# Kernel optimization log

Measured on AMD Instinct MI355X. Metric: run time of the kernel, lower is better.

## Reference

```python
import jax, jax.numpy as jnp
import numpy as np
import math

EMB_DIM = 1024
HEAD_SIZE = 64
T = 4096
B = 4

def setup_inputs() -> dict:
    key = jax.random.key(0)
    k1, k2, k3, k4 = jax.random.split(key, 4)
    scale = 1.0 / math.sqrt(EMB_DIM)
    return {
        "input": jax.random.normal(k1, (B, T, EMB_DIM), dtype=jnp.float32),
        "Wq": jax.random.normal(k2, (EMB_DIM, HEAD_SIZE), dtype=jnp.float32) * scale,
        "Wk": jax.random.normal(k3, (EMB_DIM, HEAD_SIZE), dtype=jnp.float32) * scale,
        "Wv": jax.random.normal(k4, (EMB_DIM, HEAD_SIZE), dtype=jnp.float32) * scale,
    }

def reference(input, Wq, Wk, Wv):
    # q,k,v: [B,T,H]
    q = input @ Wq
    k = input @ Wk
    v = input @ Wv
    # scores: [B,T,T]
    match = jnp.einsum('bqh,bkh->bqk', q, k)
    # 'encoder' mask in this repo = causal tril mask
    causal = jnp.tril(jnp.ones((T, T), dtype=bool))
    match = jnp.where(causal, match, -jnp.inf)
    # NOTE: faithful to source quirk: softmax first, THEN divide by sqrt(head_size)
    attention = jax.nn.softmax(match, axis=-1) / math.sqrt(HEAD_SIZE)
    return jnp.einsum('bqk,bkh->bqh', attention, v)
```

## Files before the change

### kernel.cpp

```cpp
#include <hip/hip_runtime.h>

#define T_SEQ 4096
#define NBATCH 4
#define EMB 1024
#define HS 64
#define BT (NBATCH * T_SEQ)

typedef float f32x4 __attribute__((ext_vector_type(4)));
typedef short s16x8 __attribute__((ext_vector_type(8)));

__device__ __forceinline__ unsigned short f2bf(float x) {
  union { float f; unsigned u; } c; c.f = x;
  unsigned r = c.u + 0x7FFF + ((c.u >> 16) & 1);
  return (unsigned short)(r >> 16);
}
__device__ __forceinline__ float bf2f(unsigned short h) {
  union { unsigned u; float f; } c; c.u = ((unsigned)h) << 16;
  return c.f;
}
__device__ __forceinline__ unsigned cvtpk(float lo, float hi) {
  unsigned r;
  asm("v_cvt_pk_bf16_f32 %0, %1, %2" : "=v"(r) : "v"(lo), "v"(hi));
  return r;
}
__device__ __forceinline__ void cvt8(float4 a0, float4 a1, s16x8& hi, s16x8& lo) {
  float xv[8] = {a0.x, a0.y, a0.z, a0.w, a1.x, a1.y, a1.z, a1.w};
#pragma unroll
  for (int j = 0; j < 8; ++j) {
    unsigned short h = f2bf(xv[j]);
    hi[j] = (short)h;
    lo[j] = (short)f2bf(xv[j] - bf2f(h));
  }
}
__device__ __forceinline__ void cvt8t(float4 a0, float4 a1, s16x8& hi, s16x8& lo) {
  float xv[8] = {a0.x, a0.y, a0.z, a0.w, a1.x, a1.y, a1.z, a1.w};
  unsigned hu[8], lu[8];
#pragma unroll
  for (int j = 0; j < 8; ++j) {
    union { float f; unsigned u; } c; c.f = xv[j];
    hu[j] = c.u;
    union { unsigned u; float f; } hf; hf.u = c.u & 0xFFFF0000u;
    union { float f; unsigned u; } r; r.f = xv[j] - hf.f;
    lu[j] = r.u;
  }
  union { s16x8 v; unsigned u[4]; } H, L;
#pragma unroll
  for (int j = 0; j < 4; ++j) {
    H.u[j] = (hu[2 * j] >> 16) | (hu[2 * j + 1] & 0xFFFF0000u);
    L.u[j] = (lu[2 * j] >> 16) | (lu[2 * j + 1] & 0xFFFF0000u);
  }
  hi = H.v; lo = L.v;
}

__device__ __forceinline__ void gl16(const void* g, void* l) {
  __builtin_amdgcn_global_load_lds(
      (const __attribute__((address_space(1))) void*)g,
      (__attribute__((address_space(3))) void*)l, 16, 0, 0);
}

__global__ __launch_bounds__(256) void wconv(
    const float* __restrict__ Wq, const float* __restrict__ Wk,
    const float* __restrict__ Wv, unsigned short* __restrict__ wt_hi,
    unsigned short* __restrict__ wt_lo) {
  const int n3 = blockIdx.x;
  const int which = n3 >> 6, n = n3 & 63;
  const float* W = (which == 0) ? Wq : (which == 1) ? Wk : Wv;
#pragma unroll
  for (int i = 0; i < 4; ++i) {
    int k = i * 256 + threadIdx.x;
    float x = W[(size_t)k * HS + n];
    unsigned short h = f2bf(x);
    wt_hi[(size_t)n3 * EMB + k] = h;
    wt_lo[(size_t)n3 * EMB + k] = f2bf(x - bf2f(h));
  }
}

__global__ __launch_bounds__(512) void qkv_mfma(
    const float* __restrict__ inp, const unsigned short* __restrict__ wt_hi,
    const unsigned short* __restrict__ wt_lo, float* __restrict__ qf,
    unsigned short* __restrict__ khi, unsigned short* __restrict__ klo,
    unsigned short* __restrict__ vtb) {
  __shared__ __align__(16) unsigned short S0[24576];
  __shared__ __align__(16) unsigned short S1[24576];
  const int t = threadIdx.x, lane = t & 63, w = t >> 6;
  const int m = lane & 15, quad = lane >> 4;
  const int mg = w >> 1, ng = w & 1;
  const int tok0 = blockIdx.x * 64;
  const int arow = tok0 + mg * 16 + m;

  f32x4 acc[6];
#pragma unroll
  for (int nt = 0; nt < 6; ++nt) acc[nt] = (f32x4){0.f, 0.f, 0.f, 0.f};

  const int rl = lane >> 3;
  const int cl = ((lane & 7) ^ rl) * 8;
  const unsigned short* ghi = wt_hi + (size_t)(w * 8 + rl) * EMB + cl;
  const unsigned short* glo = wt_lo + (size_t)(w * 8 + rl) * EMB + cl;
  unsigned short* const l0 = S0 + w * 512;
  unsigned short* const l1 = S1 + w * 512;

#define SB0() __builtin_amdgcn_sched_barrier(0)

#define STAGE(LB, K0)                                    \
  gl16(ghi + (K0), (LB));                                \
  gl16(ghi + 64 * EMB + (K0), (LB) + 4096);              \
  gl16(ghi + 128 * EMB + (K0), (LB) + 8192);             \
  gl16(glo + (K0), (LB) + 12288);                        \
  gl16(glo + 64 * EMB + (K0), (LB) + 16384);             \
  gl16(glo + 128 * EMB + (K0), (LB) + 20480);            \
  SB0();

#define LOAD_A(K0, PA0, PA1, PA2, PA3)                               \
  {                                                                  \
    const float* ap = &inp[(size_t)arow * EMB + (K0) + quad * 8];    \
    PA0 = *(const float4*)ap;        PA1 = *(const float4*)(ap + 4); \
    PA2 = *(const float4*)(ap + 32); PA3 = *(const float4*)(ap + 36);\
  }

#define VMBAR(N)                                                        \
  {                                                                     \
    SB0();                                                              \
    asm volatile("s_waitcnt vmcnt(" #N ") lgkmcnt(0)" ::: "memory");    \
    SB0();                                                              \
    __builtin_amdgcn_s_barrier();                                       \
  }

  const int csw0 = (quad ^ (m & 7)) * 8;
  const int csw1 = ((quad + 4) ^ (m & 7)) * 8;

#define QKV_TILE(S, AH0, AL0, AH1, AL1)                                      \
  {                                                                          \
    _Pragma("unroll")                                                        \
    for (int nt = 0; nt < 6; ++nt) {                                         \
      const int bb = (ng * 96 + nt * 16 + m) * 64;                           \
      f32x4 a = acc[nt];                                                     \
      {                                                                      \
        s16x8 bh = *(const s16x8*)&S[bb + csw0];                             \
        s16x8 bl = *(const s16x8*)&S[12288 + bb + csw0];                     \
        a = __builtin_amdgcn_mfma_f32_16x16x32_bf16(AH0, bh, a, 0, 0, 0);    \
        a = __builtin_amdgcn_mfma_f32_16x16x32_bf16(AH0, bl, a, 0, 0, 0);    \
        a = __builtin_amdgcn_mfma_f32_16x16x32_bf16(AL0, bh, a, 0, 0, 0);    \
      }                                                                      \
      {                                                                      \
        s16x8 bh = *(const s16x8*)&S[bb + csw1];                             \
        s16x8 bl = *(const s16x8*)&S[12288 + bb + csw1];                     \
        a = __builtin_amdgcn_mfma_f32_16x16x32_bf16(AH1, bh, a, 0, 0, 0);    \
        a = __builtin_amdgcn_mfma_f32_16x16x32_bf16(AH1, bl, a, 0, 0, 0);    \
        a = __builtin_amdgcn_mfma_f32_16x16x32_bf16(AL1, bh, a, 0, 0, 0);    \
      }                                                                      \
      acc[nt] = a;                                                           \
    }                                                                        \
  }

  float4 paA0, paA1, paA2, paA3;
  float4 paB0, paB1, paB2, paB3;

  STAGE(l0, 0);
  LOAD_A(0, paA0, paA1, paA2, paA3);
  LOAD_A(64, paB0, paB1, paB2, paB3);
  VMBAR(8);

#pragma unroll 1
  for (int kc = 0; kc < 8; ++kc) {
    STAGE(l1, (2 * kc + 1) * 64);
    {
      s16x8 ah0, al0, ah1, al1;
      cvt8t(paA0, paA1, ah0, al0);
      cvt8t(paA2, paA3, ah1, al1);
      if (kc < 7) { LOAD_A((2 * kc + 2) * 64, paA0, paA1, paA2, paA3); }
      QKV_TILE(S0, ah0, al0, ah1, al1);
    }
    if (kc < 7) { VMBAR(4); } else { VMBAR(0); }
    if (kc < 7) { STAGE(l0, (2 * kc + 2) * 64); }
    {
      s16x8 ah0, al0, ah1, al1;
      cvt8t(paB0, paB1, ah0, al0);
      cvt8t(paB2, paB3, ah1, al1);
      if (kc < 7) { LOAD_A((2 * kc + 3) * 64, paB0, paB1, paB2, paB3); }
      QKV_TILE(S1, ah0, al0, ah1, al1);
    }
    if (kc < 7) VMBAR(4);
  }

#undef STAGE
#undef LOAD_A
#undef QKV_TILE
#undef VMBAR
#undef SB0

#pragma unroll
  for (int nt = 0; nt < 6; ++nt) {
    int n3 = ng * 96 + nt * 16 + m;
    int which = n3 >> 6, col = n3 & 63;
#pragma unroll
    for (int r = 0; r < 4; ++r) {
      int tok = tok0 + mg * 16 + quad * 4 + r;
      float val = acc[nt][r];
      if (which == 0) {
        qf[(size_t)tok * HS + col] = val * 1.44269504088896f;
      } else if (which == 1) {
        unsigned short h = f2bf(val);
        khi[(size_t)tok * HS + col] = h;
        klo[(size_t)tok * HS + col] = f2bf(val - bf2f(h));
      } else {
        vtb[(size_t)(tok >> 6) * 4096 + (size_t)col * 64 + (tok & 63)] = f2bf(val);
      }
    }
  }
}

__global__ __launch_bounds__(256) void attn_part(
    const float* __restrict__ q, const unsigned short* __restrict__ khi,
    const unsigned short* __restrict__ klo, const unsigned short* __restrict__ vt,
    unsigned short* __restrict__ partO, float* __restrict__ partML) {
  __shared__ unsigned short Khi_s[64 * 72];
  __shared__ unsigned short Klo_s[64 * 72];
  __shared__ unsigned short Vt_s[64 * 72];
  __shared__ unsigned short P_s[4 * 16 * 72];
  const int t = threadIdx.x;
  const int lane = t & 63, w = t >> 6;
  const int m = lane & 15, quad = lane >> 4;

  int u = blockIdx.x;
  const int b = u / 160;
  u -= b * 160;
  int qtile = 0, c = 0;
  {
    int acc2 = 0;
    for (int qq = 0; qq < 64; ++qq) {
      int ncq = (qq >> 4) + 1;
      if (u < acc2 + ncq) { qtile = qq; c = u - acc2; break; }
      acc2 += ncq;
    }
  }
  const int kt0 = c * 16;
  const int kt1 = (kt0 + 16 < qtile + 1) ? kt0 + 16 : qtile + 1;

  const size_t qrow0 = (size_t)b * T_SEQ + (size_t)qtile * 64;
  const size_t krowbase = (size_t)b * T_SEQ;
  const int q_loc = w * 16 + m;

  s16x8 qh[2], ql[2];
#pragma unroll
  for (int cc = 0; cc < 2; ++cc) {
    const float* qp = &q[(qrow0 + q_loc) * HS + cc * 32 + quad * 8];
    cvt8(*(const float4*)qp, *(const float4*)(qp + 4), qh[cc], ql[cc]);
  }

  float l_st = 0.f;
  f32x4 o[4];
#pragma unroll
  for (int hb = 0; hb < 4; ++hb) o[hb] = (f32x4){0.f, 0.f, 0.f, 0.f};

  const int r0 = t >> 3, ch0 = t & 7;
  const int r1 = (256 + t) >> 3, ch1 = t & 7;

  uint4 pk0h, pk0l, pv0, pk1h, pk1l, pv1;
  {
    size_t g0 = (krowbase + (size_t)kt0 * 64 + r0) * HS + ch0 * 8;
    size_t g1 = (krowbase + (size_t)kt0 * 64 + r1) * HS + ch1 * 8;
    pk0h = *(const uint4*)&khi[g0]; pk0l = *(const uint4*)&klo[g0];
    pk1h = *(const uint4*)&khi[g1]; pk1l = *(const uint4*)&klo[g1];
    size_t v0 = (size_t)(b * 64 + kt0) * 4096 + (size_t)r0 * 64 + ch0 * 8;
    size_t v1 = (size_t)(b * 64 + kt0) * 4096 + (size_t)r1 * 64 + ch1 * 8;
    pv0 = *(const uint4*)&vt[v0]; pv1 = *(const uint4*)&vt[v1];
  }

  for (int kt = kt0; kt < kt1; ++kt) {
    __syncthreads();
    *(uint4*)&Khi_s[r0 * 72 + ch0 * 8] = pk0h;
    *(uint4*)&Klo_s[r0 * 72 + ch0 * 8] = pk0l;
    *(uint4*)&Vt_s[r0 * 72 + ch0 * 8] = pv0;
    *(uint4*)&Khi_s[r1 * 72 + ch1 * 8] = pk1h;
    *(uint4*)&Klo_s[r1 * 72 + ch1 * 8] = pk1l;
    *(uint4*)&Vt_s[r1 * 72 + ch1 * 8] = pv1;
    __syncthreads();

    if (kt + 1 < kt1) {
      size_t g0 = (krowbase + (size_t)(kt + 1) * 64 + r0) * HS + ch0 * 8;
      size_t g1 = (krowbase + (size_t)(kt + 1) * 64 + r1) * HS + ch1 * 8;
      pk0h = *(const uint4*)&khi[g0]; pk0l = *(const uint4*)&klo[g0];
      pk1h = *(const uint4*)&khi[g1]; pk1l = *(const uint4*)&klo[g1];
      size_t v0 = (size_t)(b * 64 + kt + 1) * 4096 + (size_t)r0 * 64 + ch0 * 8;
      size_t v1 = (size_t)(b * 64 + kt + 1) * 4096 + (size_t)r1 * 64 + ch1 * 8;
      pv0 = *(const uint4*)&vt[v0]; pv1 = *(const uint4*)&vt[v1];
    }

    f32x4 st[4];
#pragma unroll
    for (int cb = 0; cb < 4; ++cb) {
      st[cb] = (f32x4){0.f, 0.f, 0.f, 0.f};
#pragma unroll
      for (int cc = 0; cc < 2; ++cc) {
        s16x8 bh = *(const s16x8*)&Khi_s[(cb * 16 + m) * 72 + cc * 32 + quad * 8];
        s16x8 bl = *(const s16x8*)&Klo_s[(cb * 16 + m) * 72 + cc * 32 + quad * 8];
        st[cb] = __builtin_amdgcn_mfma_f32_16x16x32_bf16(bh, qh[cc], st[cb], 0, 0, 0);
        st[cb] = __builtin_amdgcn_mfma_f32_16x16x32_bf16(bl, qh[cc], st[cb], 0, 0, 0);
        st[cb] = __builtin_amdgcn_mfma_f32_16x16x32_bf16(bh, ql[cc], st[cb], 0, 0, 0);
      }
    }
    if (kt == qtile) {
#pragma unroll
      for (int cb = 0; cb < 4; ++cb)
#pragma unroll
        for (int r = 0; r < 4; ++r)
          if (cb * 16 + quad * 4 + r > q_loc) st[cb][r] = -1e30f;
    }
    float tc[4];
#pragma unroll
    for (int cb = 0; cb < 4; ++cb) {
#pragma unroll
      for (int r = 0; r < 4; ++r) st[cb][r] = exp2f(st[cb][r]);
      tc[cb] = (st[cb][0] + st[cb][1]) + (st[cb][2] + st[cb][3]);
    }
    l_st += (tc[0] + tc[1]) + (tc[2] + tc[3]);
#pragma unroll
    for (int cb = 0; cb < 4; ++cb) {
      uint2 pk;
      pk.x = cvtpk(st[cb][0], st[cb][1]);
      pk.y = cvtpk(st[cb][2], st[cb][3]);
      *(uint2*)&P_s[q_loc * 72 + cb * 16 + quad * 4] = pk;
    }
    s16x8 pf[2];
#pragma unroll
    for (int cc = 0; cc < 2; ++cc)
      pf[cc] = *(const s16x8*)&P_s[q_loc * 72 + cc * 32 + quad * 8];
#pragma unroll
    for (int hb = 0; hb < 4; ++hb) {
#pragma unroll
      for (int cc = 0; cc < 2; ++cc) {
        s16x8 vf = *(const s16x8*)&Vt_s[(hb * 16 + m) * 72 + cc * 32 + quad * 8];
        o[hb] = __builtin_amdgcn_mfma_f32_16x16x32_bf16(vf, pf[cc], o[hb], 0, 0, 0);
      }
    }
  }

  l_st += __shfl_xor(l_st, 16, 64);
  l_st += __shfl_xor(l_st, 32, 64);

  const int slot = ((b * 64 + qtile) << 2) + c;
  unsigned short* Op = partO + (size_t)slot * 4096;
#pragma unroll
  for (int hb = 0; hb < 4; ++hb) {
    uint2 pk;
    pk.x = cvtpk(o[hb][0], o[hb][1]);
    pk.y = cvtpk(o[hb][2], o[hb][3]);
    *(uint2*)&Op[q_loc * 64 + hb * 16 + quad * 4] = pk;
  }
  if (quad == 0) partML[(size_t)slot * 64 + q_loc] = l_st;
}

__global__ __launch_bounds__(256) void attn_combine(
    const unsigned short* __restrict__ partO, const float* __restrict__ partML,
    float* __restrict__ out) {
  const int qtile = blockIdx.x, b = blockIdx.y;
  const int t = threadIdx.x;
  const int row = t >> 2, hg = t & 3;
  const int nc = (qtile >> 4) + 1;
  const int slot0 = (b * 64 + qtile) << 2;

  float lsum = 0.f;
  for (int i = 0; i < nc; ++i) lsum += partML[(size_t)(slot0 + i) * 64 + row];
  const float inv = 1.f / (lsum * 8.0f);

  float acc[16];
#pragma unroll
  for (int e = 0; e < 16; ++e) acc[e] = 0.f;
  for (int i = 0; i < nc; ++i) {
    const unsigned short* Op =
        partO + (size_t)(slot0 + i) * 4096 + row * 64 + hg * 16;
    uint4 u0 = *(const uint4*)Op;
    uint4 u1 = *(const uint4*)(Op + 8);
    unsigned uv[8] = {u0.x, u0.y, u0.z, u0.w, u1.x, u1.y, u1.z, u1.w};
#pragma unroll
    for (int e = 0; e < 8; ++e) {
      acc[2 * e] += bf2f((unsigned short)(uv[e] & 0xFFFF));
      acc[2 * e + 1] += bf2f((unsigned short)(uv[e] >> 16));
    }
  }
  float* op = &out[((size_t)b * T_SEQ + (size_t)qtile * 64 + row) * HS + hg * 16];
#pragma unroll
  for (int v = 0; v < 4; ++v) {
    float4 r;
    r.x = acc[4 * v + 0] * inv; r.y = acc[4 * v + 1] * inv;
    r.z = acc[4 * v + 2] * inv; r.w = acc[4 * v + 3] * inv;
    ((float4*)op)[v] = r;
  }
}

extern "C" void kernel_launch(void* const* d_in, const int* in_sizes, int n_in,
                              void* d_out, int out_size, void* d_ws, size_t ws_size,
                              hipStream_t stream) {
  const float* inp = (const float*)d_in[0];
  const float* Wq  = (const float*)d_in[1];
  const float* Wk  = (const float*)d_in[2];
  const float* Wv  = (const float*)d_in[3];
  float* out = (float*)d_out;

  char* base = (char*)d_ws;
  float* qf = (float*)base;
  unsigned short* khi = (unsigned short*)(base + (size_t)BT * HS * 4);
  unsigned short* klo = khi + (size_t)BT * HS;
  unsigned short* vtb = klo + (size_t)BT * HS;
  unsigned short* wt_hi = vtb + (size_t)BT * HS;
  unsigned short* wt_lo = wt_hi + (size_t)192 * EMB;
  unsigned short* partO = wt_lo + (size_t)192 * EMB;
  float* partML = (float*)(partO + (size_t)1024 * 4096);

  wconv<<<dim3(192), dim3(256), 0, stream>>>(Wq, Wk, Wv, wt_hi, wt_lo);
  qkv_mfma<<<dim3(BT / 64), dim3(512), 0, stream>>>(inp, wt_hi, wt_lo, qf, khi, klo, vtb);
  attn_part<<<dim3(640), dim3(256), 0, stream>>>(qf, khi, klo, vtb, partO, partML);
  attn_combine<<<dim3(64, NBATCH), dim3(256), 0, stream>>>(partO, partML, out);
}
```

Before: 166.0 us.

## Double-buffer K/V tiles in LDS via direct global-to-LDS loads with XOR swizzle

Replaces the register-staged single LDS buffer with two LDS buffers filled by direct global-to-LDS loads (gl16). The next tile is prefetched while the current one is computed, and each step needs only one barrier instead of two. The padded layout becomes an XOR-swizzled layout to avoid bank conflicts, and blocks are launched in reverse order so the heavy causal tiles start first. LDS use roughly doubles, which may lower occupancy, and the correctness of the swizzle and the ordering relies on sched_barrier placement.

```diff
diff --git a/kernel.cpp b/kernel.cpp
--- a/kernel.cpp
+++ b/kernel.cpp
@@ -213,15 +213,14 @@
     const float* __restrict__ q, const unsigned short* __restrict__ khi,
     const unsigned short* __restrict__ klo, const unsigned short* __restrict__ vt,
     unsigned short* __restrict__ partO, float* __restrict__ partML) {
-  __shared__ unsigned short Khi_s[64 * 72];
-  __shared__ unsigned short Klo_s[64 * 72];
-  __shared__ unsigned short Vt_s[64 * 72];
+  __shared__ __align__(16) unsigned short S0[12288];
+  __shared__ __align__(16) unsigned short S1[12288];
   __shared__ unsigned short P_s[4 * 16 * 72];
   const int t = threadIdx.x;
   const int lane = t & 63, w = t >> 6;
   const int m = lane & 15, quad = lane >> 4;
 
-  int u = blockIdx.x;
+  int u = (int)gridDim.x - 1 - blockIdx.x;
   const int b = u / 160;
   u -= b * 160;
   int qtile = 0, c = 0;
@@ -252,88 +251,115 @@
 #pragma unroll
   for (int hb = 0; hb < 4; ++hb) o[hb] = (f32x4){0.f, 0.f, 0.f, 0.f};
 
-  const int r0 = t >> 3, ch0 = t & 7;
-  const int r1 = (256 + t) >> 3, ch1 = t & 7;
-
-  uint4 pk0h, pk0l, pv0, pk1h, pk1l, pv1;
-  {
-    size_t g0 = (krowbase + (size_t)kt0 * 64 + r0) * HS + ch0 * 8;
-    size_t g1 = (krowbase + (size_t)kt0 * 64 + r1) * HS + ch1 * 8;
-    pk0h = *(const uint4*)&khi[g0]; pk0l = *(const uint4*)&klo[g0];
-    pk1h = *(const uint4*)&khi[g1]; pk1l = *(const uint4*)&klo[g1];
-    size_t v0 = (size_t)(b * 64 + kt0) * 4096 + (size_t)r0 * 64 + ch0 * 8;
-    size_t v1 = (size_t)(b * 64 + kt0) * 4096 + (size_t)r1 * 64 + ch1 * 8;
-    pv0 = *(const uint4*)&vt[v0]; pv1 = *(const uint4*)&vt[v1];
-  }
-
-  for (int kt = kt0; kt < kt1; ++kt) {
-    __syncthreads();
-    *(uint4*)&Khi_s[r0 * 72 + ch0 * 8] = pk0h;
-    *(uint4*)&Klo_s[r0 * 72 + ch0 * 8] = pk0l;
-    *(uint4*)&Vt_s[r0 * 72 + ch0 * 8] = pv0;
-    *(uint4*)&Khi_s[r1 * 72 + ch1 * 8] = pk1h;
-    *(uint4*)&Klo_s[r1 * 72 + ch1 * 8] = pk1l;
-    *(uint4*)&Vt_s[r1 * 72 + ch1 * 8] = pv1;
-    __syncthreads();
-
+  const int lro = lane >> 3;
+  const int lcs = ((lane & 7) ^ lro) * 8;
+  const int rloc = w * 16 + lro;
+  const unsigned short* pkh = khi + (krowbase + rloc) * HS + lcs;
+  const unsigned short* pkl = klo + (krowbase + rloc) * HS + lcs;
+  const unsigned short* pvt = vt + (size_t)(b * 64) * 4096 + rloc * 64 + lcs;
+
+#define SB0() __builtin_amdgcn_sched_barrier(0)
+#define STAGE(SB, KT)                                        \
+  {                                                          \
+    const size_t o_ = (size_t)(KT) * 4096;                   \
+    gl16(pkh + o_,       (SB) + w * 1024);                   \
+    gl16(pkh + o_ + 512, (SB) + w * 1024 + 512);             \
+    gl16(pkl + o_,       (SB) + 4096 + w * 1024);            \
+    gl16(pkl + o_ + 512, (SB) + 4096 + w * 1024 + 512);      \
+    gl16(pvt + o_,       (SB) + 8192 + w * 1024);            \
+    gl16(pvt + o_ + 512, (SB) + 8192 + w * 1024 + 512);      \
+    SB0();                                                   \
+  }
+#define VMBAR0()                                                      \
+  {                                                                   \
+    SB0();                                                            \
+    asm volatile("s_waitcnt vmcnt(0) lgkmcnt(0)" ::: "memory");       \
+    SB0();                                                            \
+    __builtin_amdgcn_s_barrier();                                     \
+  }
+
+  const int rc0 = ((quad)     ^ (m & 7)) * 8;
+  const int rc1 = ((quad + 4) ^ (m & 7)) * 8;
+
+#define ACOMPUTE(SB, KT)                                                       \
+  {                                                                            \
+    f32x4 st[4];                                                               \
+    _Pragma("unroll")                                                          \
+    for (int cb = 0; cb < 4; ++cb) {                                           \
+      st[cb] = (f32x4){0.f, 0.f, 0.f, 0.f};                                    \
+      const int rb = (cb * 16 + m) * 64;                                       \
+      {                                                                        \
+        s16x8 bh = *(const s16x8*)&(SB)[rb + rc0];                             \
+        s16x8 bl = *(const s16x8*)&(SB)[4096 + rb + rc0];                      \
+        st[cb] = __builtin_amdgcn_mfma_f32_16x16x32_bf16(bh, qh[0], st[cb], 0, 0, 0); \
+        st[cb] = __builtin_amdgcn_mfma_f32_16x16x32_bf16(bl, qh[0], st[cb], 0, 0, 0); \
+        st[cb] = __builtin_amdgcn_mfma_f32_16x16x32_bf16(bh, ql[0], st[cb], 0, 0, 0); \
+      }                                                                        \
+      {                                                                        \
+        s16x8 bh = *(const s16x8*)&(SB)[rb + rc1];                             \
+        s16x8 bl = *(const s16x8*)&(SB)[4096 + rb + rc1];                      \
+        st[cb] = __builtin_amdgcn_mfma_f32_16x16x32_bf16(bh, qh[1], st[cb], 0, 0, 0); \
+        st[cb] = __builtin_amdgcn_mfma_f32_16x16x32_bf16(bl, qh[1], st[cb], 0, 0, 0); \
+        st[cb] = __builtin_amdgcn_mfma_f32_16x16x32_bf16(bh, ql[1], st[cb], 0, 0, 0); \
+      }                                                                        \
+    }                                                                          \
+    if ((KT) == qtile) {                                                       \
+      _Pragma("unroll")                                                        \
+      for (int cb = 0; cb < 4; ++cb)                                           \
+        _Pragma("unroll")                                                      \
+        for (int r = 0; r < 4; ++r)                                            \
+          if (cb * 16 + quad * 4 + r > q_loc) st[cb][r] = -1e30f;              \
+    }                                                                          \
+    float tc[4];                                                               \
+    _Pragma("unroll")                                                          \
+    for (int cb = 0; cb < 4; ++cb) {                                           \
+      _Pragma("unroll")                                                        \
+      for (int r = 0; r < 4; ++r) st[cb][r] = exp2f(st[cb][r]);                \
+      tc[cb] = (st[cb][0] + st[cb][1]) + (st[cb][2] + st[cb][3]);              \
+    }                                                                          \
+    l_st += (tc[0] + tc[1]) + (tc[2] + tc[3]);                                 \
+    _Pragma("unroll")                                                          \
+    for (int cb = 0; cb < 4; ++cb) {                                           \
+      uint2 pk;                                                                \
+      pk.x = cvtpk(st[cb][0], st[cb][1]);                                      \
+      pk.y = cvtpk(st[cb][2], st[cb][3]);                                      \
+      *(uint2*)&P_s[q_loc * 72 + cb * 16 + quad * 4] = pk;                     \
+    }                                                                          \
+    s16x8 pf0 = *(const s16x8*)&P_s[q_loc * 72 + quad * 8];                    \
+    s16x8 pf1 = *(const s16x8*)&P_s[q_loc * 72 + 32 + quad * 8];               \
+    _Pragma("unroll")                                                          \
+    for (int hb = 0; hb < 4; ++hb) {                                           \
+      const int vb = (hb * 16 + m) * 64;                                       \
+      {                                                                        \
+        s16x8 vf = *(const s16x8*)&(SB)[8192 + vb + rc0];                      \
+        o[hb] = __builtin_amdgcn_mfma_f32_16x16x32_bf16(vf, pf0, o[hb], 0, 0, 0); \
+      }                                                                        \
+      {                                                                        \
+        s16x8 vf = *(const s16x8*)&(SB)[8192 + vb + rc1];                      \
+        o[hb] = __builtin_amdgcn_mfma_f32_16x16x32_bf16(vf, pf1, o[hb], 0, 0, 0); \
+      }                                                                        \
+    }                                                                          \
+  }
+
+  STAGE(S0, kt0);
+  VMBAR0();
+
+#pragma unroll 1
+  for (int kt = kt0; kt < kt1; kt += 2) {
+    if (kt + 1 < kt1) STAGE(S1, kt + 1);
+    ACOMPUTE(S0, kt);
+    VMBAR0();
     if (kt + 1 < kt1) {
-      size_t g0 = (krowbase + (size_t)(kt + 1) * 64 + r0) * HS + ch0 * 8;
-      size_t g1 = (krowbase + (size_t)(kt + 1) * 64 + r1) * HS + ch1 * 8;
-      pk0h = *(const uint4*)&khi[g0]; pk0l = *(const uint4*)&klo[g0];
-      pk1h = *(const uint4*)&khi[g1]; pk1l = *(const uint4*)&klo[g1];
-      size_t v0 = (size_t)(b * 64 + kt + 1) * 4096 + (size_t)r0 * 64 + ch0 * 8;
-      size_t v1 = (size_t)(b * 64 + kt + 1) * 4096 + (size_t)r1 * 64 + ch1 * 8;
-      pv0 = *(const uint4*)&vt[v0]; pv1 = *(const uint4*)&vt[v1];
-    }
-
-    f32x4 st[4];
-#pragma unroll
-    for (int cb = 0; cb < 4; ++cb) {
-      st[cb] = (f32x4){0.f, 0.f, 0.f, 0.f};
-#pragma unroll
-      for (int cc = 0; cc < 2; ++cc) {
-        s16x8 bh = *(const s16x8*)&Khi_s[(cb * 16 + m) * 72 + cc * 32 + quad * 8];
-        s16x8 bl = *(const s16x8*)&Klo_s[(cb * 16 + m) * 72 + cc * 32 + quad * 8];
-        st[cb] = __builtin_amdgcn_mfma_f32_16x16x32_bf16(bh, qh[cc], st[cb], 0, 0, 0);
-        st[cb] = __builtin_amdgcn_mfma_f32_16x16x32_bf16(bl, qh[cc], st[cb], 0, 0, 0);
-        st[cb] = __builtin_amdgcn_mfma_f32_16x16x32_bf16(bh, ql[cc], st[cb], 0, 0, 0);
-      }
-    }
-    if (kt == qtile) {
-#pragma unroll
-      for (int cb = 0; cb < 4; ++cb)
-#pragma unroll
-        for (int r = 0; r < 4; ++r)
-          if (cb * 16 + quad * 4 + r > q_loc) st[cb][r] = -1e30f;
-    }
-    float tc[4];
-#pragma unroll
-    for (int cb = 0; cb < 4; ++cb) {
-#pragma unroll
-      for (int r = 0; r < 4; ++r) st[cb][r] = exp2f(st[cb][r]);
-      tc[cb] = (st[cb][0] + st[cb][1]) + (st[cb][2] + st[cb][3]);
-    }
-    l_st += (tc[0] + tc[1]) + (tc[2] + tc[3]);
-#pragma unroll
-    for (int cb = 0; cb < 4; ++cb) {
-      uint2 pk;
-      pk.x = cvtpk(st[cb][0], st[cb][1]);
-      pk.y = cvtpk(st[cb][2], st[cb][3]);
-      *(uint2*)&P_s[q_loc * 72 + cb * 16 + quad * 4] = pk;
-    }
-    s16x8 pf[2];
-#pragma unroll
-    for (int cc = 0; cc < 2; ++cc)
-      pf[cc] = *(const s16x8*)&P_s[q_loc * 72 + cc * 32 + quad * 8];
-#pragma unroll
-    for (int hb = 0; hb < 4; ++hb) {
-#pragma unroll
-      for (int cc = 0; cc < 2; ++cc) {
-        s16x8 vf = *(const s16x8*)&Vt_s[(hb * 16 + m) * 72 + cc * 32 + quad * 8];
-        o[hb] = __builtin_amdgcn_mfma_f32_16x16x32_bf16(vf, pf[cc], o[hb], 0, 0, 0);
-      }
-    }
-  }
+      if (kt + 2 < kt1) STAGE(S0, kt + 2);
+      ACOMPUTE(S1, kt + 1);
+      VMBAR0();
+    }
+  }
+
+#undef STAGE
+#undef VMBAR0
+#undef ACOMPUTE
+#undef SB0
 
   l_st += __shfl_xor(l_st, 16, 64);
   l_st += __shfl_xor(l_st, 32, 64);
```

After: 173.2 us. +4.4%, slower.

## Enlarge attention query tile to 128 rows with 512-thread blocks

Applied to the files above, without the earlier changes.

Doubles the query rows per attention block from 64 to 128 using 8 waves, so each K/V tile staged in shared memory is reused by twice as many queries. Grid shrinks from 640 to 320 blocks, and the combine kernel is adapted to the new partial layout. This halves K/V global and LDS load traffic per query, at the cost of fewer blocks, coarser causal load balance, and a second masked diagonal tile per block.

```diff
diff --git a/kernel.cpp b/kernel.cpp
--- a/kernel.cpp
+++ b/kernel.cpp
@@ -209,34 +209,35 @@
   }
 }
 
-__global__ __launch_bounds__(256) void attn_part(
+__global__ __launch_bounds__(512) void attn_part(
     const float* __restrict__ q, const unsigned short* __restrict__ khi,
     const unsigned short* __restrict__ klo, const unsigned short* __restrict__ vt,
     unsigned short* __restrict__ partO, float* __restrict__ partML) {
   __shared__ unsigned short Khi_s[64 * 72];
   __shared__ unsigned short Klo_s[64 * 72];
   __shared__ unsigned short Vt_s[64 * 72];
-  __shared__ unsigned short P_s[4 * 16 * 72];
+  __shared__ unsigned short P_s[128 * 72];
   const int t = threadIdx.x;
   const int lane = t & 63, w = t >> 6;
   const int m = lane & 15, quad = lane >> 4;
 
   int u = blockIdx.x;
-  const int b = u / 160;
-  u -= b * 160;
+  const int b = u / 80;
+  u -= b * 80;
   int qtile = 0, c = 0;
   {
     int acc2 = 0;
-    for (int qq = 0; qq < 64; ++qq) {
-      int ncq = (qq >> 4) + 1;
+    for (int qq = 0; qq < 32; ++qq) {
+      int ncq = (qq >> 3) + 1;
       if (u < acc2 + ncq) { qtile = qq; c = u - acc2; break; }
       acc2 += ncq;
     }
   }
+  const int nkt = 2 * qtile + 2;
   const int kt0 = c * 16;
-  const int kt1 = (kt0 + 16 < qtile + 1) ? kt0 + 16 : qtile + 1;
-
-  const size_t qrow0 = (size_t)b * T_SEQ + (size_t)qtile * 64;
+  const int kt1 = (kt0 + 16 < nkt) ? kt0 + 16 : nkt;
+
+  const size_t qrow0 = (size_t)b * T_SEQ + (size_t)qtile * 128;
   const size_t krowbase = (size_t)b * T_SEQ;
   const int q_loc = w * 16 + m;
 
@@ -253,37 +254,29 @@
   for (int hb = 0; hb < 4; ++hb) o[hb] = (f32x4){0.f, 0.f, 0.f, 0.f};
 
   const int r0 = t >> 3, ch0 = t & 7;
-  const int r1 = (256 + t) >> 3, ch1 = t & 7;
-
-  uint4 pk0h, pk0l, pv0, pk1h, pk1l, pv1;
+
+  uint4 pkh, pkl, pv;
   {
     size_t g0 = (krowbase + (size_t)kt0 * 64 + r0) * HS + ch0 * 8;
-    size_t g1 = (krowbase + (size_t)kt0 * 64 + r1) * HS + ch1 * 8;
-    pk0h = *(const uint4*)&khi[g0]; pk0l = *(const uint4*)&klo[g0];
-    pk1h = *(const uint4*)&khi[g1]; pk1l = *(const uint4*)&klo[g1];
+    pkh = *(const uint4*)&khi[g0];
+    pkl = *(const uint4*)&klo[g0];
     size_t v0 = (size_t)(b * 64 + kt0) * 4096 + (size_t)r0 * 64 + ch0 * 8;
-    size_t v1 = (size_t)(b * 64 + kt0) * 4096 + (size_t)r1 * 64 + ch1 * 8;
-    pv0 = *(const uint4*)&vt[v0]; pv1 = *(const uint4*)&vt[v1];
+    pv = *(const uint4*)&vt[v0];
   }
 
   for (int kt = kt0; kt < kt1; ++kt) {
     __syncthreads();
-    *(uint4*)&Khi_s[r0 * 72 + ch0 * 8] = pk0h;
-    *(uint4*)&Klo_s[r0 * 72 + ch0 * 8] = pk0l;
-    *(uint4*)&Vt_s[r0 * 72 + ch0 * 8] = pv0;
-    *(uint4*)&Khi_s[r1 * 72 + ch1 * 8] = pk1h;
-    *(uint4*)&Klo_s[r1 * 72 + ch1 * 8] = pk1l;
-    *(uint4*)&Vt_s[r1 * 72 + ch1 * 8] = pv1;
+    *(uint4*)&Khi_s[r0 * 72 + ch0 * 8] = pkh;
+    *(uint4*)&Klo_s[r0 * 72 + ch0 * 8] = pkl;
+    *(uint4*)&Vt_s[r0 * 72 + ch0 * 8] = pv;
     __syncthreads();
 
     if (kt + 1 < kt1) {
       size_t g0 = (krowbase + (size_t)(kt + 1) * 64 + r0) * HS + ch0 * 8;
-      size_t g1 = (krowbase + (size_t)(kt + 1) * 64 + r1) * HS + ch1 * 8;
-      pk0h = *(const uint4*)&khi[g0]; pk0l = *(const uint4*)&klo[g0];
-      pk1h = *(const uint4*)&khi[g1]; pk1l = *(const uint4*)&klo[g1];
+      pkh = *(const uint4*)&khi[g0];
+      pkl = *(const uint4*)&klo[g0];
       size_t v0 = (size_t)(b * 64 + kt + 1) * 4096 + (size_t)r0 * 64 + ch0 * 8;
-      size_t v1 = (size_t)(b * 64 + kt + 1) * 4096 + (size_t)r1 * 64 + ch1 * 8;
-      pv0 = *(const uint4*)&vt[v0]; pv1 = *(const uint4*)&vt[v1];
+      pv = *(const uint4*)&vt[v0];
     }
 
     f32x4 st[4];
@@ -299,12 +292,14 @@
         st[cb] = __builtin_amdgcn_mfma_f32_16x16x32_bf16(bh, ql[cc], st[cb], 0, 0, 0);
       }
     }
-    if (kt == qtile) {
+    const int dkt = kt - 2 * qtile;
+    if (dkt >= 0) {
+      const int qrel = q_loc - dkt * 64;
 #pragma unroll
       for (int cb = 0; cb < 4; ++cb)
 #pragma unroll
         for (int r = 0; r < 4; ++r)
-          if (cb * 16 + quad * 4 + r > q_loc) st[cb][r] = -1e30f;
+          if (cb * 16 + quad * 4 + r > qrel) st[cb][r] = -1e30f;
     }
     float tc[4];
 #pragma unroll
@@ -338,8 +333,8 @@
   l_st += __shfl_xor(l_st, 16, 64);
   l_st += __shfl_xor(l_st, 32, 64);
 
-  const int slot = ((b * 64 + qtile) << 2) + c;
-  unsigned short* Op = partO + (size_t)slot * 4096;
+  const int slot = ((b * 32 + qtile) << 2) + c;
+  unsigned short* Op = partO + (size_t)slot * 8192;
 #pragma unroll
   for (int hb = 0; hb < 4; ++hb) {
     uint2 pk;
@@ -347,7 +342,7 @@
     pk.y = cvtpk(o[hb][2], o[hb][3]);
     *(uint2*)&Op[q_loc * 64 + hb * 16 + quad * 4] = pk;
   }
-  if (quad == 0) partML[(size_t)slot * 64 + q_loc] = l_st;
+  if (quad == 0) partML[(size_t)slot * 128 + q_loc] = l_st;
 }
 
 __global__ __launch_bounds__(256) void attn_combine(
@@ -355,32 +350,34 @@
     float* __restrict__ out) {
   const int qtile = blockIdx.x, b = blockIdx.y;
   const int t = threadIdx.x;
-  const int row = t >> 2, hg = t & 3;
-  const int nc = (qtile >> 4) + 1;
-  const int slot0 = (b * 64 + qtile) << 2;
+  const int row = t >> 1, half = t & 1;
+  const int nc = (qtile >> 3) + 1;
+  const int slot0 = (b * 32 + qtile) << 2;
 
   float lsum = 0.f;
-  for (int i = 0; i < nc; ++i) lsum += partML[(size_t)(slot0 + i) * 64 + row];
+  for (int i = 0; i < nc; ++i) lsum += partML[(size_t)(slot0 + i) * 128 + row];
   const float inv = 1.f / (lsum * 8.0f);
 
-  float acc[16];
-#pragma unroll
-  for (int e = 0; e < 16; ++e) acc[e] = 0.f;
+  float acc[32];
+#pragma unroll
+  for (int e = 0; e < 32; ++e) acc[e] = 0.f;
   for (int i = 0; i < nc; ++i) {
     const unsigned short* Op =
-        partO + (size_t)(slot0 + i) * 4096 + row * 64 + hg * 16;
-    uint4 u0 = *(const uint4*)Op;
-    uint4 u1 = *(const uint4*)(Op + 8);
-    unsigned uv[8] = {u0.x, u0.y, u0.z, u0.w, u1.x, u1.y, u1.z, u1.w};
-#pragma unroll
-    for (int e = 0; e < 8; ++e) {
-      acc[2 * e] += bf2f((unsigned short)(uv[e] & 0xFFFF));
-      acc[2 * e + 1] += bf2f((unsigned short)(uv[e] >> 16));
-    }
-  }
-  float* op = &out[((size_t)b * T_SEQ + (size_t)qtile * 64 + row) * HS + hg * 16];
-#pragma unroll
-  for (int v = 0; v < 4; ++v) {
+        partO + (size_t)(slot0 + i) * 8192 + row * 64 + half * 32;
+#pragma unroll
+    for (int v = 0; v < 4; ++v) {
+      uint4 u0 = *(const uint4*)(Op + v * 8);
+      unsigned uv[4] = {u0.x, u0.y, u0.z, u0.w};
+#pragma unroll
+      for (int e = 0; e < 4; ++e) {
+        acc[v * 8 + 2 * e] += bf2f((unsigned short)(uv[e] & 0xFFFF));
+        acc[v * 8 + 2 * e + 1] += bf2f((unsigned short)(uv[e] >> 16));
+      }
+    }
+  }
+  float* op = &out[((size_t)b * T_SEQ + (size_t)qtile * 128 + row) * HS + half * 32];
+#pragma unroll
+  for (int v = 0; v < 8; ++v) {
     float4 r;
     r.x = acc[4 * v + 0] * inv; r.y = acc[4 * v + 1] * inv;
     r.z = acc[4 * v + 2] * inv; r.w = acc[4 * v + 3] * inv;
@@ -405,10 +402,10 @@
   unsigned short* wt_hi = vtb + (size_t)BT * HS;
   unsigned short* wt_lo = wt_hi + (size_t)192 * EMB;
   unsigned short* partO = wt_lo + (size_t)192 * EMB;
-  float* partML = (float*)(partO + (size_t)1024 * 4096);
+  float* partML = (float*)(partO + (size_t)512 * 8192);
 
   wconv<<<dim3(192), dim3(256), 0, stream>>>(Wq, Wk, Wv, wt_hi, wt_lo);
   qkv_mfma<<<dim3(BT / 64), dim3(512), 0, stream>>>(inp, wt_hi, wt_lo, qf, khi, klo, vtb);
-  attn_part<<<dim3(640), dim3(256), 0, stream>>>(qf, khi, klo, vtb, partO, partML);
-  attn_combine<<<dim3(64, NBATCH), dim3(256), 0, stream>>>(partO, partML, out);
-}
+  attn_part<<<dim3(320), dim3(512), 0, stream>>>(qf, khi, klo, vtb, partO, partML);
+  attn_combine<<<dim3(32, NBATCH), dim3(256), 0, stream>>>(partO, partML, out);
+}
```

Result: slower. 172.2 us (+3.8%).
